# Optimization experiments

Hardware: AMD Instinct MI355X
Metric: run time of the kernel (lower is better)

## Reference

```python
import jax, jax.numpy as jnp
import numpy as np

N = 100000      # nodes
E = 1600000     # edges (avg degree 16)
N_IN, N_HID, N_OUT = 512, 256, 64
HOP = 10


def setup_inputs() -> dict:
    key = jax.random.key(0)
    k = jax.random.split(key, 8)
    x = jax.random.normal(k[0], (N, N_IN), dtype=jnp.float32)
    edge_row = jax.random.randint(k[1], (E,), 0, N, dtype=jnp.int64)
    edge_col = jax.random.randint(k[2], (E,), 0, N, dtype=jnp.int64)
    # values ~ 1/avg_degree, mimicking normalized adjacency
    edge_vals = jax.random.uniform(k[3], (E,), dtype=jnp.float32) * 0.0625
    W1 = jax.random.normal(k[4], (N_HID, N_IN), dtype=jnp.float32) * (1.0 / np.sqrt(N_IN))
    b1 = jnp.zeros((N_HID,), dtype=jnp.float32)
    W2 = jax.random.normal(k[5], (N_OUT, N_HID), dtype=jnp.float32) * (1.0 / np.sqrt(N_HID))
    b2 = jnp.zeros((N_OUT,), dtype=jnp.float32)
    s = jax.random.normal(k[6], (N_OUT, 1), dtype=jnp.float32) * 0.1
    return {"x": x, "edge_row": edge_row, "edge_col": edge_col,
            "edge_vals": edge_vals, "W1": W1, "b1": b1, "W2": W2,
            "b2": b2, "s": s}


def reference(x, edge_row, edge_col, edge_vals, W1, b1, W2, b2, s):
    # MLP transform (dropout=0 / eval mode)
    h = jax.nn.relu(x @ W1.T + b1)          # [N, N_HID]
    h = h @ W2.T + b2                        # [N, N_OUT]
    # multi-hop sparse propagation: h_{k+1} = A @ h_k  (COO SpMM)
    outs = [h]
    for _ in range(HOP):
        msg = edge_vals[:, None] * h[edge_col]                       # [E, N_OUT]
        h = jax.ops.segment_sum(msg, edge_row, num_segments=N)       # [N, N_OUT]
        outs.append(h)
    H = jnp.stack(outs, axis=1)              # [N, HOP+1, N_OUT]
    # sigmoid hop-attention: S = sigmoid(H @ s), out = S^T H
    S = jax.nn.sigmoid(jnp.einsum('nkf,fo->nk', H, s))  # [N, HOP+1]
    out = jnp.einsum('nk,nkf->nf', S, H)     # [N, N_OUT]
    return out
```

## Files before the change

kernel.cpp:

```cpp
#include <hip/hip_runtime.h>
#include <hip/hip_bf16.h>

#define NIN  512
#define NHID 256
#define NOUT 64
#define HOPS 10

typedef __attribute__((ext_vector_type(8))) short bf16x8;
typedef __attribute__((ext_vector_type(4))) float f32x4;

__device__ __forceinline__ unsigned short f2bf(float f) {
    unsigned u = __float_as_uint(f);
    u += 0x7FFFu + ((u >> 16) & 1u);
    return (unsigned short)(u >> 16);
}
__device__ __forceinline__ unsigned pk2(float a, float b) {
    return (unsigned)f2bf(a) | ((unsigned)f2bf(b) << 16);
}
__device__ __forceinline__ float bflo(unsigned g) { return __uint_as_float(g << 16); }
__device__ __forceinline__ float bfhi(unsigned g) { return __uint_as_float(g & 0xFFFF0000u); }

__global__ void k_preconv(const float* __restrict__ W1, const float* __restrict__ W2,
                          unsigned short* __restrict__ W1f, unsigned short* __restrict__ W2f)
{
    const int i = blockIdx.x * 256 + threadIdx.x;
    if (i < NHID * NIN) {
        const int j = i & 7, l = (i >> 3) & 63, fi = i >> 9;
        const int ks = fi >> 4, w = (fi >> 2) & 3, nf = fi & 3;
        const int col = w * 64 + nf * 16 + (l & 15);
        const int k   = ks * 32 + ((l >> 4) << 3) + j;
        W1f[i] = f2bf(W1[col * NIN + k]);
    }
    if (i < NOUT * NHID) {
        const int j = i & 7, l = (i >> 3) & 63, fi = i >> 9;
        const int ks = fi >> 2, nf = fi & 3;
        const int col = nf * 16 + (l & 15);
        const int k   = ks * 32 + ((j >> 2) << 4) + ((l >> 4) << 2) + (j & 3);
        W2f[i] = f2bf(W2[col * NHID + k]);
    }
}

__global__ __launch_bounds__(256, 3) void mlp_kernel(
    const float* __restrict__ x, const unsigned short* __restrict__ W1f,
    const float* __restrict__ b1, const unsigned short* __restrict__ W2f,
    const float* __restrict__ b2,
    unsigned* __restrict__ hpack, int n)
{
    __shared__ __align__(16) char smem[50176];
    short* B2L  = (short*)smem;
    short* BX   = (short*)(smem + 32768);
    float* H0L  = (float*)(smem + 32768);

    const int t  = threadIdx.x;
    const int w  = t >> 6, lz = t & 63;
    const int row0 = blockIdx.x * 64;

    const int srow = t >> 2;
    int xrow = row0 + srow; if (xrow >= n) xrow = n - 1;
    const float4* xp = (const float4*)(x + (size_t)xrow * NIN);
    const int q4a = t & 3, q4b = (t & 3) + 4;

    f32x4 acc[4][4];
    #pragma unroll
    for (int a = 0; a < 4; ++a)
        #pragma unroll
        for (int b = 0; b < 4; ++b) acc[a][b] = (f32x4)(0.f);

    auto xwrite = [&](int b, float4 va, float4 vb) {
        unsigned long long pa = (unsigned long long)pk2(va.x, va.y)
                              | ((unsigned long long)pk2(va.z, va.w) << 32);
        unsigned long long pb = (unsigned long long)pk2(vb.x, vb.y)
                              | ((unsigned long long)pk2(vb.z, vb.w) << 32);
        *(unsigned long long*)&BX[(((((b << 2) + (srow >> 4)) << 6)
            + ((srow & 15) | ((q4a >> 1) << 4))) << 3) + ((q4a & 1) << 2)] = pa;
        *(unsigned long long*)&BX[(((((b << 2) + (srow >> 4)) << 6)
            + ((srow & 15) | ((q4b >> 1) << 4))) << 3) + ((q4b & 1) << 2)] = pb;
    };
    auto wload = [&](int kt, bf16x8* wf) {
        const unsigned short* wp = W1f + ((size_t)kt << 13) + (w << 11) + (lz << 3);
        #pragma unroll
        for (int hf = 0; hf < 4; ++hf)
            wf[hf] = *(const bf16x8*)(wp + (hf << 9));
    };
    auto compute = [&](int b, const bf16x8* wf) {
        bf16x8 xf[4];
        #pragma unroll
        for (int nfn = 0; nfn < 4; ++nfn)
            xf[nfn] = *(const bf16x8*)&BX[((((b << 2) + nfn) << 6) + lz) << 3];
        #pragma unroll
        for (int nfn = 0; nfn < 4; ++nfn)
            #pragma unroll
            for (int hf = 0; hf < 4; ++hf)
                acc[nfn][hf] = __builtin_amdgcn_mfma_f32_16x16x32_bf16(
                    wf[hf], xf[nfn], acc[nfn][hf], 0, 0, 0);
    };

    bf16x8 wfc[4], wfn[4];
    float4 sAa, sAb, sBa, sBb;
    {
        float4 xa = xp[q4a], xb = xp[q4b];
        wload(0, wfc);
        xwrite(0, xa, xb);
        sAa = xp[8 + q4a]; sAb = xp[8 + q4b];
    }
    __syncthreads();

    #pragma unroll 1
    for (int kt = 0; kt < 16; kt += 2) {
        if (kt + 2 < 16) { sBa = xp[((kt + 2) << 3) + q4a]; sBb = xp[((kt + 2) << 3) + q4b]; }
        wload(kt + 1, wfn);
        compute(0, wfc);
        xwrite(1, sAa, sAb);
        __syncthreads();
        if (kt + 3 < 16) { sAa = xp[((kt + 3) << 3) + q4a]; sAb = xp[((kt + 3) << 3) + q4b]; }
        if (kt + 2 < 16) wload(kt + 2, wfc);
        compute(1, wfn);
        if (kt + 2 < 16) xwrite(0, sBa, sBb);
        __syncthreads();
    }

    {
        float4 b1q[4];
        #pragma unroll
        for (int hf = 0; hf < 4; ++hf)
            b1q[hf] = *(const float4*)(b1 + (w << 6) + (hf << 4) + ((lz >> 4) << 2));
        #pragma unroll
        for (int nfn = 0; nfn < 4; ++nfn) {
            #pragma unroll
            for (int cl = 0; cl < 2; ++cl) {
                f32x4 a0 = acc[nfn][2 * cl], a1 = acc[nfn][2 * cl + 1];
                float4 c0 = b1q[2 * cl], c1 = b1q[2 * cl + 1];
                uint4 pv;
                pv.x = pk2(fmaxf(a0.x + c0.x, 0.f), fmaxf(a0.y + c0.y, 0.f));
                pv.y = pk2(fmaxf(a0.z + c0.z, 0.f), fmaxf(a0.w + c0.w, 0.f));
                pv.z = pk2(fmaxf(a1.x + c1.x, 0.f), fmaxf(a1.y + c1.y, 0.f));
                pv.w = pk2(fmaxf(a1.z + c1.z, 0.f), fmaxf(a1.w + c1.w, 0.f));
                *(uint4*)&B2L[((((nfn << 3) + (w << 1) + cl) << 6) + lz) << 3] = pv;
            }
        }
    }
    __syncthreads();

    f32x4 acc2[4];
    #pragma unroll
    for (int nf2 = 0; nf2 < 4; ++nf2) acc2[nf2] = (f32x4)(0.f);

    #pragma unroll
    for (int c = 0; c < 8; ++c) {
        bf16x8 hfrag = *(const bf16x8*)&B2L[((((w << 3) + c) << 6) + lz) << 3];
        #pragma unroll
        for (int nf2 = 0; nf2 < 4; ++nf2) {
            bf16x8 wfrag = *(const bf16x8*)(W2f + (((c << 2) + nf2) << 9) + (lz << 3));
            acc2[nf2] = __builtin_amdgcn_mfma_f32_16x16x32_bf16(
                wfrag, hfrag, acc2[nf2], 0, 0, 0);
        }
    }

    {
        const int mloc = (w << 4) + (lz & 15);
        #pragma unroll
        for (int nf2 = 0; nf2 < 4; ++nf2) {
            float4 bq = *(const float4*)(b2 + (nf2 << 4) + ((lz >> 4) << 2));
            float4 hv;
            hv.x = acc2[nf2].x + bq.x; hv.y = acc2[nf2].y + bq.y;
            hv.z = acc2[nf2].z + bq.z; hv.w = acc2[nf2].w + bq.w;
            *(float4*)&H0L[mloc * 68 + (nf2 << 4) + ((lz >> 4) << 2)] = hv;
        }
    }
    __syncthreads();

    {
        const int m = t >> 2, q = t & 3;
        const int g = row0 + m;
        if (g < n) {
            unsigned* hp = hpack + (size_t)g * 32 + (q << 3);
            #pragma unroll
            for (int i = 0; i < 16; i += 4) {
                float4 hv = *(const float4*)&H0L[m * 68 + (q << 4) + i];
                uint2 pv;
                pv.x = pk2(hv.x, hv.y);
                pv.y = pk2(hv.z, hv.w);
                *(uint2*)(hp + (i >> 1)) = pv;
            }
        }
    }
}

__global__ __launch_bounds__(256) void kA_hist(
    const int* __restrict__ erow, int* __restrict__ bcnt, int e, int nbk)
{
    __shared__ int lh[512];
    const int t = threadIdx.x;
    for (int b = t; b < 512; b += 256) lh[b] = 0;
    __syncthreads();
    for (int i = blockIdx.x * 256 + t; i < e; i += gridDim.x * 256)
        atomicAdd(&lh[erow[i] >> 8], 1);
    __syncthreads();
    for (int b = t; b < nbk; b += 256)
        if (lh[b]) atomicAdd(&bcnt[b], lh[b]);
}

__global__ __launch_bounds__(512) void kB_scan(
    const int* __restrict__ bcnt, int* __restrict__ bbase,
    int* __restrict__ gcur, int e, int nbk)
{
    __shared__ int sm[512];
    const int tid = threadIdx.x;
    const int v = (tid < nbk) ? bcnt[tid] : 0;
    sm[tid] = v;
    __syncthreads();
    for (int off = 1; off < 512; off <<= 1) {
        int tv = (tid >= off) ? sm[tid - off] : 0;
        __syncthreads();
        sm[tid] += tv;
        __syncthreads();
    }
    if (tid < nbk) {
        const int base = sm[tid] - v;
        bbase[tid] = base;
        gcur[tid * 16] = base;
    }
    if (tid == 0) bbase[nbk] = e;
}

__global__ __launch_bounds__(256) void k_bapp(
    const int* __restrict__ erow, const int* __restrict__ ecol,
    const float* __restrict__ ev, int* __restrict__ gcur,
    uint4* __restrict__ brec, int e, int nbk)
{
    __shared__ int lh[512];
    __shared__ int lbase[512];
    const int t = threadIdx.x;
    const int c0 = blockIdx.x * 4096;
    for (int b = t; b < 512; b += 256) lh[b] = 0;
    __syncthreads();
    int rr[16];
    #pragma unroll
    for (int j = 0; j < 16; ++j) {
        const int i = c0 + j * 256 + t;
        rr[j] = (i < e) ? erow[i] : -1;
        if (rr[j] >= 0) atomicAdd(&lh[rr[j] >> 8], 1);
    }
    __syncthreads();
    for (int b = t; b < nbk; b += 256) {
        const int c = lh[b];
        lbase[b] = c ? atomicAdd(&gcur[b * 16], c) : 0;
        lh[b] = 0;
    }
    __syncthreads();
    #pragma unroll
    for (int j = 0; j < 16; ++j) {
        const int i = c0 + j * 256 + t;
        if (rr[j] >= 0) {
            const int b  = rr[j] >> 8;
            const int rk = atomicAdd(&lh[b], 1);
            uint4 rec;
            rec.x = (unsigned)rr[j];
            rec.y = (unsigned)ecol[i];
            rec.z = __float_as_uint(ev[i]);
            rec.w = 0;
            brec[lbase[b] + rk] = rec;
        }
    }
}

__global__ __launch_bounds__(256) void k_brow(
    const uint4* __restrict__ brec, const int* __restrict__ bbase,
    int* __restrict__ rp, int n, int e)
{
    __shared__ int rc[256];
    __shared__ int sc[256];
    const int b = blockIdx.x, t = threadIdx.x;
    const int lo = bbase[b], hi = bbase[b + 1];
    rc[t] = 0;
    __syncthreads();
    for (int i = lo + t; i < hi; i += 256) {
        const unsigned r = ((const unsigned*)brec)[(size_t)i * 4];
        atomicAdd(&rc[r & 255], 1);
    }
    __syncthreads();
    const int v = rc[t];
    sc[t] = v;
    __syncthreads();
    for (int off = 1; off < 256; off <<= 1) {
        int tv = (t >= off) ? sc[t - off] : 0;
        __syncthreads();
        sc[t] += tv;
        __syncthreads();
    }
    const int row = (b << 8) + t;
    if (row < n) rp[row] = lo + sc[t] - v;
    if (b == 0 && t == 0) rp[n] = e;
}

__global__ __launch_bounds__(256) void k_bwrite(
    const uint4* __restrict__ brec, const int* __restrict__ bbase,
    const int* __restrict__ rp, unsigned long long* __restrict__ cpack)
{
    __shared__ int rc[256];
    const int b = blockIdx.x, t = threadIdx.x;
    const int lo = bbase[b], hi = bbase[b + 1];
    rc[t] = 0;
    __syncthreads();
    for (int i = lo + t; i < hi; i += 256) {
        const uint4 rec = brec[i];
        const int rk = atomicAdd(&rc[rec.x & 255], 1);
        cpack[rp[rec.x] + rk] = ((unsigned long long)rec.z << 32) | rec.y;
    }
}

__global__ __launch_bounds__(256) void hop_kernel(
    const unsigned* __restrict__ h_in, unsigned* __restrict__ h_out,
    const int* __restrict__ row_ptr, const unsigned long long* __restrict__ cpack,
    int n)
{
    const int t  = threadIdx.x;
    const int sl = t & 31;
    const int node = (blockIdx.x * 256 + t) >> 5;
    if (node >= n) return;
    const int start = row_ptr[node];
    const int end   = row_ptr[node + 1];
    float a0 = 0.f, a1 = 0.f;
    for (int base = start; base < end; base += 32) {
        const int idx = base + sl;
        unsigned long long pc = (idx < end) ? cpack[idx] : 0ULL;
        int   c = (int)(unsigned)pc;
        float v = __uint_as_float((unsigned)(pc >> 32));
        const int cnt = min(32, end - base);
        int e = 0;
        for (; e + 8 <= cnt; e += 8) {
            int cc[8]; float vv[8]; unsigned gg[8];
            #pragma unroll
            for (int j = 0; j < 8; ++j) {
                cc[j] = __shfl(c, e + j, 32);
                vv[j] = __shfl(v, e + j, 32);
            }
            #pragma unroll
            for (int j = 0; j < 8; ++j)
                gg[j] = h_in[(size_t)cc[j] * 32 + sl];
            #pragma unroll
            for (int j = 0; j < 8; ++j) {
                a0 = fmaf(vv[j], bflo(gg[j]), a0);
                a1 = fmaf(vv[j], bfhi(gg[j]), a1);
            }
        }
        for (; e + 4 <= cnt; e += 4) {
            int cc[4]; float vv[4]; unsigned gg[4];
            #pragma unroll
            for (int j = 0; j < 4; ++j) {
                cc[j] = __shfl(c, e + j, 32);
                vv[j] = __shfl(v, e + j, 32);
            }
            #pragma unroll
            for (int j = 0; j < 4; ++j)
                gg[j] = h_in[(size_t)cc[j] * 32 + sl];
            #pragma unroll
            for (int j = 0; j < 4; ++j) {
                a0 = fmaf(vv[j], bflo(gg[j]), a0);
                a1 = fmaf(vv[j], bfhi(gg[j]), a1);
            }
        }
        for (; e < cnt; ++e) {
            int   cc = __shfl(c, e, 32);
            float vv = __shfl(v, e, 32);
            unsigned g = h_in[(size_t)cc * 32 + sl];
            a0 = fmaf(vv, bflo(g), a0); a1 = fmaf(vv, bfhi(g), a1);
        }
    }
    h_out[(size_t)node * 32 + sl] = pk2(a0, a1);
}

__global__ __launch_bounds__(256) void k_combine(
    const unsigned* __restrict__ hbuf, const float* __restrict__ s,
    float* __restrict__ out, int n)
{
    const int gid  = blockIdx.x * 256 + threadIdx.x;
    const int node = gid >> 5, sl = gid & 31;
    if (node >= n) return;
    const float2 sv = ((const float2*)s)[sl];
    float o0 = 0.f, o1 = 0.f;
    #pragma unroll
    for (int k = 0; k <= HOPS; ++k) {
        const unsigned g = hbuf[(size_t)k * n * 32 + (size_t)node * 32 + sl];
        const float lo = bflo(g), hi = bfhi(g);
        float tv = lo * sv.x + hi * sv.y;
        #pragma unroll
        for (int off = 16; off > 0; off >>= 1) tv += __shfl_xor(tv, off, 32);
        const float sg = 1.f / (1.f + expf(-tv));
        o0 = fmaf(sg, lo, o0);
        o1 = fmaf(sg, hi, o1);
    }
    float2 ov; ov.x = o0; ov.y = o1;
    ((float2*)out)[(size_t)node * 32 + sl] = ov;
}

extern "C" void kernel_launch(void* const* d_in, const int* in_sizes, int n_in,
                              void* d_out, int out_size, void* d_ws, size_t ws_size,
                              hipStream_t stream)
{
    const float* x  = (const float*)d_in[0];
    const int*   er = (const int*)  d_in[1];
    const int*   ec = (const int*)  d_in[2];
    const float* ev = (const float*)d_in[3];
    const float* W1 = (const float*)d_in[4];
    const float* b1 = (const float*)d_in[5];
    const float* W2 = (const float*)d_in[6];
    const float* b2 = (const float*)d_in[7];
    const float* s  = (const float*)d_in[8];
    float* out = (float*)d_out;

    const int n = in_sizes[0] / NIN;
    const int e = in_sizes[1];
    const int nbk = (n + 255) >> 8;

    char* w = (char*)d_ws;
    auto carve = [&](size_t bytes) { char* p = w; w += (bytes + 255) & ~(size_t)255; return p; };
    unsigned* hbuf   = (unsigned*)carve((size_t)(HOPS + 1) * n * 32 * 4);
    int*      rp     = (int*)     carve(((size_t)n + 1) * 4);
    unsigned long long* cpack = (unsigned long long*)carve((size_t)e * 8);
    uint4*    brec   = (uint4*)   carve((size_t)e * 16);
    int*      bcnt   = (int*)     carve(512 * 4);
    int*      bbase  = (int*)     carve(513 * 4);
    int*      gcur   = (int*)     carve(512 * 16 * 4);
    unsigned short* W1f = (unsigned short*)carve((size_t)NHID * NIN * 2);
    unsigned short* W2f = (unsigned short*)carve((size_t)NOUT * NHID * 2);

    hipMemsetAsync(bcnt, 0, 512 * 4, stream);

    k_preconv<<<(NHID * NIN + 255) / 256, 256, 0, stream>>>(W1, W2, W1f, W2f);

    const int mgrid = (n + 63) / 64;
    mlp_kernel<<<mgrid, 256, 0, stream>>>(x, W1f, b1, W2f, b2, hbuf, n);

    kA_hist <<<256, 256, 0, stream>>>(er, bcnt, e, nbk);
    kB_scan <<<1, 512, 0, stream>>>(bcnt, bbase, gcur, e, nbk);
    k_bapp  <<<(e + 4095) / 4096, 256, 0, stream>>>(er, ec, ev, gcur, brec, e, nbk);
    k_brow  <<<nbk, 256, 0, stream>>>(brec, bbase, rp, n, e);
    k_bwrite<<<nbk, 256, 0, stream>>>(brec, bbase, rp, cpack);

    const int hgrid = ((size_t)n * 32 + 255) / 256;
    for (int hop = 0; hop < HOPS; ++hop) {
        hop_kernel<<<hgrid, 256, 0, stream>>>(
            hbuf + (size_t)hop * n * 32, hbuf + (size_t)(hop + 1) * n * 32,
            rp, cpack, n);
    }

    k_combine<<<hgrid, 256, 0, stream>>>(hbuf, s, out, n);
}
```

Before: 512.8 us.

## Double K-tile depth in MLP pipeline and split bucket records into SoA arrays

The MLP GEMM loop now stages 64-wide K tiles (two MFMA k-subtiles) per LDS buffer, so it runs half as many iterations and barriers. x is prefetched two tiles ahead, and W1 fragments are loaded inside compute rather than prefetched. Separately, the 16-byte bucket records (which carried a padding word) are split into a row array and a col/val pair array. This cuts traffic in the bucketing kernels, and the row-count pass now reads only 4 bytes per edge. The risks are more register pressure from the deeper x prefetch and exposed W1 load latency, since those loads are no longer prefetched.

Result: slower. 530.6 us (+3.5%).

```diff
diff --git a/kernel.cpp b/kernel.cpp
--- a/kernel.cpp
+++ b/kernel.cpp
@@ -58,7 +58,7 @@
     const int srow = t >> 2;
     int xrow = row0 + srow; if (xrow >= n) xrow = n - 1;
     const float4* xp = (const float4*)(x + (size_t)xrow * NIN);
-    const int q4a = t & 3, q4b = (t & 3) + 4;
+    const int q0 = t & 3;
 
     f32x4 acc[4][4];
     #pragma unroll
@@ -66,56 +66,55 @@
         #pragma unroll
         for (int b = 0; b < 4; ++b) acc[a][b] = (f32x4)(0.f);
 
-    auto xwrite = [&](int b, float4 va, float4 vb) {
-        unsigned long long pa = (unsigned long long)pk2(va.x, va.y)
-                              | ((unsigned long long)pk2(va.z, va.w) << 32);
-        unsigned long long pb = (unsigned long long)pk2(vb.x, vb.y)
-                              | ((unsigned long long)pk2(vb.z, vb.w) << 32);
-        *(unsigned long long*)&BX[(((((b << 2) + (srow >> 4)) << 6)
-            + ((srow & 15) | ((q4a >> 1) << 4))) << 3) + ((q4a & 1) << 2)] = pa;
-        *(unsigned long long*)&BX[(((((b << 2) + (srow >> 4)) << 6)
-            + ((srow & 15) | ((q4b >> 1) << 4))) << 3) + ((q4b & 1) << 2)] = pb;
+    auto xwq = [&](int b, float4 v, int q) {
+        unsigned long long p = (unsigned long long)pk2(v.x, v.y)
+                             | ((unsigned long long)pk2(v.z, v.w) << 32);
+        const int f   = ((q >> 3) << 2) + (srow >> 4);
+        const int row = (srow & 15) | (((q & 7) >> 1) << 4);
+        *(unsigned long long*)&BX[(((((b << 3) + f) << 6) + row) << 3) + ((q & 1) << 2)] = p;
     };
-    auto wload = [&](int kt, bf16x8* wf) {
-        const unsigned short* wp = W1f + ((size_t)kt << 13) + (w << 11) + (lz << 3);
-        #pragma unroll
-        for (int hf = 0; hf < 4; ++hf)
-            wf[hf] = *(const bf16x8*)(wp + (hf << 9));
+    auto compute = [&](int b, int kt) {
+        #pragma unroll
+        for (int ksub = 0; ksub < 2; ++ksub) {
+            bf16x8 wf[4], xf[4];
+            const unsigned short* wp = W1f + ((size_t)(2 * kt + ksub) << 13)
+                                     + (w << 11) + (lz << 3);
+            #pragma unroll
+            for (int hf = 0; hf < 4; ++hf)
+                wf[hf] = *(const bf16x8*)(wp + (hf << 9));
+            #pragma unroll
+            for (int nfn = 0; nfn < 4; ++nfn)
+                xf[nfn] = *(const bf16x8*)&BX[((((b << 3) + (ksub << 2) + nfn) << 6) + lz) << 3];
+            #pragma unroll
+            for (int nfn = 0; nfn < 4; ++nfn)
+                #pragma unroll
+                for (int hf = 0; hf < 4; ++hf)
+                    acc[nfn][hf] = __builtin_amdgcn_mfma_f32_16x16x32_bf16(
+                        wf[hf], xf[nfn], acc[nfn][hf], 0, 0, 0);
+        }
     };
-    auto compute = [&](int b, const bf16x8* wf) {
-        bf16x8 xf[4];
-        #pragma unroll
-        for (int nfn = 0; nfn < 4; ++nfn)
-            xf[nfn] = *(const bf16x8*)&BX[((((b << 2) + nfn) << 6) + lz) << 3];
-        #pragma unroll
-        for (int nfn = 0; nfn < 4; ++nfn)
-            #pragma unroll
-            for (int hf = 0; hf < 4; ++hf)
-                acc[nfn][hf] = __builtin_amdgcn_mfma_f32_16x16x32_bf16(
-                    wf[hf], xf[nfn], acc[nfn][hf], 0, 0, 0);
-    };
-
-    bf16x8 wfc[4], wfn[4];
-    float4 sAa, sAb, sBa, sBb;
-    {
-        float4 xa = xp[q4a], xb = xp[q4b];
-        wload(0, wfc);
-        xwrite(0, xa, xb);
-        sAa = xp[8 + q4a]; sAb = xp[8 + q4b];
-    }
+
+    float4 C0, C1, C2, C3, P0, P1, P2, P3, N0, N1, N2, N3;
+    C0 = xp[q0]; C1 = xp[q0 + 4]; C2 = xp[q0 + 8]; C3 = xp[q0 + 12];
+    xwq(0, C0, q0); xwq(0, C1, q0 + 4); xwq(0, C2, q0 + 8); xwq(0, C3, q0 + 12);
+    P0 = xp[16 + q0]; P1 = xp[16 + q0 + 4];
+    P2 = xp[16 + q0 + 8]; P3 = xp[16 + q0 + 12];
     __syncthreads();
 
     #pragma unroll 1
-    for (int kt = 0; kt < 16; kt += 2) {
-        if (kt + 2 < 16) { sBa = xp[((kt + 2) << 3) + q4a]; sBb = xp[((kt + 2) << 3) + q4b]; }
-        wload(kt + 1, wfn);
-        compute(0, wfc);
-        xwrite(1, sAa, sAb);
-        __syncthreads();
-        if (kt + 3 < 16) { sAa = xp[((kt + 3) << 3) + q4a]; sAb = xp[((kt + 3) << 3) + q4b]; }
-        if (kt + 2 < 16) wload(kt + 2, wfc);
-        compute(1, wfn);
-        if (kt + 2 < 16) xwrite(0, sBa, sBb);
+    for (int kt = 0; kt < 8; ++kt) {
+        const int b = kt & 1;
+        if (kt + 2 < 8) {
+            const int o = (kt + 2) << 4;
+            N0 = xp[o + q0]; N1 = xp[o + q0 + 4];
+            N2 = xp[o + q0 + 8]; N3 = xp[o + q0 + 12];
+        }
+        compute(b, kt);
+        if (kt + 1 < 8) {
+            xwq(b ^ 1, P0, q0); xwq(b ^ 1, P1, q0 + 4);
+            xwq(b ^ 1, P2, q0 + 8); xwq(b ^ 1, P3, q0 + 12);
+        }
+        if (kt + 2 < 8) { P0 = N0; P1 = N1; P2 = N2; P3 = N3; }
         __syncthreads();
     }
 
@@ -226,7 +225,7 @@
 __global__ __launch_bounds__(256) void k_bapp(
     const int* __restrict__ erow, const int* __restrict__ ecol,
     const float* __restrict__ ev, int* __restrict__ gcur,
-    uint4* __restrict__ brec, int e, int nbk)
+    unsigned* __restrict__ brow, uint2* __restrict__ bcv, int e, int nbk)
 {
     __shared__ int lh[512];
     __shared__ int lbase[512];
@@ -254,18 +253,16 @@
         if (rr[j] >= 0) {
             const int b  = rr[j] >> 8;
             const int rk = atomicAdd(&lh[b], 1);
-            uint4 rec;
-            rec.x = (unsigned)rr[j];
-            rec.y = (unsigned)ecol[i];
-            rec.z = __float_as_uint(ev[i]);
-            rec.w = 0;
-            brec[lbase[b] + rk] = rec;
+            const int pos = lbase[b] + rk;
+            brow[pos] = (unsigned)rr[j];
+            uint2 cv; cv.x = (unsigned)ecol[i]; cv.y = __float_as_uint(ev[i]);
+            bcv[pos] = cv;
         }
     }
 }
 
 __global__ __launch_bounds__(256) void k_brow(
-    const uint4* __restrict__ brec, const int* __restrict__ bbase,
+    const unsigned* __restrict__ brow, const int* __restrict__ bbase,
     int* __restrict__ rp, int n, int e)
 {
     __shared__ int rc[256];
@@ -274,10 +271,8 @@
     const int lo = bbase[b], hi = bbase[b + 1];
     rc[t] = 0;
     __syncthreads();
-    for (int i = lo + t; i < hi; i += 256) {
-        const unsigned r = ((const unsigned*)brec)[(size_t)i * 4];
-        atomicAdd(&rc[r & 255], 1);
-    }
+    for (int i = lo + t; i < hi; i += 256)
+        atomicAdd(&rc[brow[i] & 255], 1);
     __syncthreads();
     const int v = rc[t];
     sc[t] = v;
@@ -294,8 +289,9 @@
 }
 
 __global__ __launch_bounds__(256) void k_bwrite(
-    const uint4* __restrict__ brec, const int* __restrict__ bbase,
-    const int* __restrict__ rp, unsigned long long* __restrict__ cpack)
+    const unsigned* __restrict__ brow, const uint2* __restrict__ bcv,
+    const int* __restrict__ bbase, const int* __restrict__ rp,
+    unsigned long long* __restrict__ cpack)
 {
     __shared__ int rc[256];
     const int b = blockIdx.x, t = threadIdx.x;
@@ -303,9 +299,10 @@
     rc[t] = 0;
     __syncthreads();
     for (int i = lo + t; i < hi; i += 256) {
-        const uint4 rec = brec[i];
-        const int rk = atomicAdd(&rc[rec.x & 255], 1);
-        cpack[rp[rec.x] + rk] = ((unsigned long long)rec.z << 32) | rec.y;
+        const unsigned r = brow[i];
+        const uint2 cv = bcv[i];
+        const int rk = atomicAdd(&rc[r & 255], 1);
+        cpack[rp[r] + rk] = ((unsigned long long)cv.y << 32) | cv.x;
     }
 }
 
@@ -418,7 +415,8 @@
     unsigned* hbuf   = (unsigned*)carve((size_t)(HOPS + 1) * n * 32 * 4);
     int*      rp     = (int*)     carve(((size_t)n + 1) * 4);
     unsigned long long* cpack = (unsigned long long*)carve((size_t)e * 8);
-    uint4*    brec   = (uint4*)   carve((size_t)e * 16);
+    unsigned* brow   = (unsigned*)carve((size_t)e * 4);
+    uint2*    bcv    = (uint2*)   carve((size_t)e * 8);
     int*      bcnt   = (int*)     carve(512 * 4);
     int*      bbase  = (int*)     carve(513 * 4);
     int*      gcur   = (int*)     carve(512 * 16 * 4);
@@ -434,9 +432,9 @@
 
     kA_hist <<<256, 256, 0, stream>>>(er, bcnt, e, nbk);
     kB_scan <<<1, 512, 0, stream>>>(bcnt, bbase, gcur, e, nbk);
-    k_bapp  <<<(e + 4095) / 4096, 256, 0, stream>>>(er, ec, ev, gcur, brec, e, nbk);
-    k_brow  <<<nbk, 256, 0, stream>>>(brec, bbase, rp, n, e);
-    k_bwrite<<<nbk, 256, 0, stream>>>(brec, bbase, rp, cpack);
+    k_bapp  <<<(e + 4095) / 4096, 256, 0, stream>>>(er, ec, ev, gcur, brow, bcv, e, nbk);
+    k_brow  <<<nbk, 256, 0, stream>>>(brow, bbase, rp, n, e);
+    k_bwrite<<<nbk, 256, 0, stream>>>(brow, bcv, bbase, rp, cpack);
 
     const int hgrid = ((size_t)n * 32 + 255) / 256;
     for (int hop = 0; hop < HOPS; ++hop) {
```
